# Kernel optimization log

Hardware: AMD Instinct MI355X
Metric: run time of the kernel (lower is better)

## Reference

```python
import jax, jax.numpy as jnp
import numpy as np
import math

EMBED_DIM = 1024
NUM_HEADS = 16
HEAD_DIM = EMBED_DIM // NUM_HEADS
WINDOW_SIZE = 32  # one-sided; full window = 2*w+1 = 65
SCALING = math.sqrt(HEAD_DIM)


def setup_inputs() -> dict:
    key = jax.random.key(0)
    ks = jax.random.split(key, 9)
    B, S, E = 2, 2048, EMBED_DIM
    s = 1.0 / math.sqrt(E)
    inp = {
        "hidden_states": jax.random.normal(ks[0], (B, S, E), dtype=jnp.float32),
        "q_w": jax.random.uniform(ks[1], (E, E), jnp.float32, -s, s),
        "q_b": jax.random.uniform(ks[2], (E,), jnp.float32, -s, s),
        "k_w": jax.random.uniform(ks[3], (E, E), jnp.float32, -s, s),
        "k_b": jax.random.uniform(ks[4], (E,), jnp.float32, -s, s),
        "v_w": jax.random.uniform(ks[5], (E, E), jnp.float32, -s, s),
        "v_b": jax.random.uniform(ks[6], (E,), jnp.float32, -s, s),
        "o_w": jax.random.uniform(ks[7], (E, E), jnp.float32, -s, s),
        "o_b": jax.random.uniform(ks[8], (E,), jnp.float32, -s, s),
    }
    return inp


def reference(hidden_states, q_w, q_b, k_w, k_b, v_w, v_b, o_w, o_b):
    B, S, E = hidden_states.shape
    H, D, w = NUM_HEADS, HEAD_DIM, WINDOW_SIZE
    W = 2 * w + 1

    q = hidden_states @ q_w.T + q_b
    k = hidden_states @ k_w.T + k_b
    v = hidden_states @ v_w.T + v_b

    # [B, H, S, D]
    q = q.reshape(B, S, H, D).transpose(0, 2, 1, 3)
    k = k.reshape(B, S, H, D).transpose(0, 2, 1, 3)
    v = v.reshape(B, S, H, D).transpose(0, 2, 1, 3)

    # zero-pad seq dim by w on each side (matches F.pad value=0); padded keys
    # contribute score 0 (NOT -inf) exactly like the original unfold scheme.
    k_pad = jnp.pad(k, ((0, 0), (0, 0), (w, w), (0, 0)))
    v_pad = jnp.pad(v, ((0, 0), (0, 0), (w, w), (0, 0)))

    # window gather indices: query i sees padded positions i..i+2w (orig i-w..i+w)
    idx = jnp.arange(S)[:, None] + jnp.arange(W)[None, :]  # [S, W]
    k_slice = k_pad[:, :, idx]  # [B, H, S, W, D]
    v_slice = v_pad[:, :, idx]  # [B, H, S, W, D]

    score = jnp.einsum('bhsd,bhswd->bhsw', q, k_slice) / SCALING
    p = jax.nn.softmax(score, axis=-1)
    attn = jnp.einsum('bhsw,bhswd->bhsd', p, v_slice)

    attn = attn.transpose(0, 2, 1, 3).reshape(B, S, E)
    return attn @ o_w.T + o_b
```

## Files before the change

kernel.cpp:

```cpp
#include <hip/hip_runtime.h>
#include <math.h>

typedef _Float16 h16;
typedef _Float16 h8 __attribute__((ext_vector_type(8)));
typedef float f32x4 __attribute__((ext_vector_type(4)));

__device__ inline void gl2lds16(const void* g, void* l) {
  __builtin_amdgcn_global_load_lds(
      (const __attribute__((address_space(1))) void*)g,
      (__attribute__((address_space(3))) void*)l, 16, 0, 0);
}

#define VMCNT(N) asm volatile("s_waitcnt vmcnt(" #N ")" ::: "memory")

__global__ __launch_bounds__(256) void f2h_all(
    const float* __restrict__ hs, const float* __restrict__ w0,
    const float* __restrict__ w1, const float* __restrict__ w2,
    const float* __restrict__ w3, h16* __restrict__ dst, int hsN) {
  int i = (blockIdx.x * 256 + threadIdx.x) * 8;
  const int tot = hsN + 4 * 1048576;
  if (i >= tot) return;
  const float* src;
  int off;
  if (i < hsN) {
    src = hs; off = i;
  } else {
    int k = i - hsN;
    int seg = k >> 20;
    off = k & 1048575;
    src = seg == 0 ? w0 : seg == 1 ? w1 : seg == 2 ? w2 : w3;
  }
  float4 a = *(const float4*)(src + off);
  float4 b = *(const float4*)(src + off + 4);
  h8 o;
  o[0] = (h16)a.x; o[1] = (h16)a.y; o[2] = (h16)a.z; o[3] = (h16)a.w;
  o[4] = (h16)b.x; o[5] = (h16)b.y; o[6] = (h16)b.z; o[7] = (h16)b.w;
  *(h8*)(dst + i) = o;
}

__global__ __launch_bounds__(256) void qkv97(
    const h16* __restrict__ A, const h16* __restrict__ Bw,
    const float* __restrict__ qb, const float* __restrict__ kb,
    const float* __restrict__ vb, h16* __restrict__ qo, h16* __restrict__ ko,
    h16* __restrict__ vo) {
  __shared__ __align__(16) h16 Ash[128 * 32];
  __shared__ __align__(16) h16 Bsh[128 * 32];
  __shared__ __align__(16) h16 Csh[128 * 136];

  const int tid = threadIdx.x;
  const int wid = tid >> 6, lane = tid & 63;
  const int lr = lane & 15, lg = lane >> 4;
  const int wr = wid >> 1, wc = wid & 1;
  const int srow = tid >> 2;
  const int csw = ((tid & 3) ^ ((srow >> 1) & 3)) * 8;

  const int wg = (blockIdx.x & 7) * 96 + (blockIdx.x >> 3);
  const int bm = wg & 31, bn = wg >> 5;
  const int row0 = bm * 128, col0 = bn * 128;

  const h16* Ag = A + (size_t)row0 * 1024;
  const h16* Bg = Bw + (size_t)col0 * 1024;

  auto ldf = [&](const h16* base, int row) -> h8 {
    return *(const h8*)(base + row * 32 + (lg ^ ((row >> 1) & 3)) * 8);
  };

  f32x4 acc[4][4] = {};

  for (int t = 0; t < 32; ++t) {
    const int kof = t * 32 + csw;
    gl2lds16(Ag + (size_t)srow * 1024 + kof, &Ash[(wid * 16) * 32]);
    gl2lds16(Ag + (size_t)(64 + srow) * 1024 + kof, &Ash[(64 + wid * 16) * 32]);
    gl2lds16(Bg + (size_t)srow * 1024 + kof, &Bsh[(wid * 16) * 32]);
    gl2lds16(Bg + (size_t)(64 + srow) * 1024 + kof, &Bsh[(64 + wid * 16) * 32]);
    __syncthreads();
    h8 af[4], bf[4];
#pragma unroll
    for (int m = 0; m < 4; ++m) af[m] = ldf(Ash, wr * 64 + m * 16 + lr);
#pragma unroll
    for (int n = 0; n < 4; ++n) bf[n] = ldf(Bsh, wc * 64 + n * 16 + lr);
    __builtin_amdgcn_s_setprio(1);
#pragma unroll
    for (int m = 0; m < 4; ++m)
#pragma unroll
      for (int n = 0; n < 4; ++n)
        acc[m][n] =
            __builtin_amdgcn_mfma_f32_16x16x32_f16(af[m], bf[n], acc[m][n], 0, 0, 0);
    __builtin_amdgcn_s_setprio(0);
    __syncthreads();
  }

  const int tsel = bn >> 3;
  const int colseg = (bn & 7) * 128;
  const float* bp = tsel == 0 ? qb : (tsel == 1 ? kb : vb);
  h16* outp = tsel == 0 ? qo : (tsel == 1 ? ko : vo);

#pragma unroll
  for (int n = 0; n < 4; ++n) {
    const int ccol = wc * 64 + n * 16 + lr;
    const float bv = bp[colseg + ccol];
#pragma unroll
    for (int m = 0; m < 4; ++m)
#pragma unroll
      for (int j = 0; j < 4; ++j)
        Csh[(wr * 64 + m * 16 + lg * 4 + j) * 136 + ccol] =
            (h16)(acc[m][n][j] + bv);
  }
  __syncthreads();
#pragma unroll
  for (int p = 0; p < 8; ++p) {
    const int idx = p * 256 + tid;
    const int r = idx >> 4, c = idx & 15;
    h8 v = *(const h8*)&Csh[r * 136 + c * 8];
    *(h8*)&outp[(size_t)(row0 + r) * 1024 + colseg + c * 8] = v;
  }
}

__global__ __launch_bounds__(64) void oproj1w(const h16* __restrict__ A,
                                              const h16* __restrict__ Bw,
                                              const float* __restrict__ b0,
                                              float* __restrict__ Cf) {
  __shared__ __align__(16) h16 Ash[2][32][64];
  __shared__ __align__(16) h16 Bsh[2][128][64];

  const int lane = threadIdx.x;
  const int lr = lane & 15, lg = lane >> 4;
  const int srw = lane >> 3;
  const int csw = ((lane & 7) ^ (srw & 7)) * 8;

  const int wg = (blockIdx.x & 7) * 128 + (blockIdx.x >> 3);
  const int bm = wg & 127, bn = wg >> 7;
  const int row0 = bm * 32, col0 = bn * 128;

  const h16* Ag = A + (size_t)row0 * 1024;
  const h16* Bg = Bw + (size_t)col0 * 1024;

  auto stage = [&](int t, int bi) {
    const int kof = t * 64 + csw;
#pragma unroll
    for (int rs = 0; rs < 32; rs += 8)
      gl2lds16(Ag + (size_t)(rs + srw) * 1024 + kof, &Ash[bi][rs][0]);
#pragma unroll
    for (int rs = 0; rs < 128; rs += 8)
      gl2lds16(Bg + (size_t)(rs + srw) * 1024 + kof, &Bsh[bi][rs][0]);
  };
  auto ldf = [&](const h16* base, int row, int kk) -> h8 {
    return *(const h8*)(base + row * 64 + ((kk * 4 + lg) ^ (row & 7)) * 8);
  };

  f32x4 acc[2][8] = {};

  stage(0, 0);
  for (int t = 0; t < 16; ++t) {
    if (t + 1 < 16) {
      stage(t + 1, (t + 1) & 1);
      VMCNT(20);
    } else {
      VMCNT(0);
    }
    const h16* Ar = &Ash[t & 1][0][0];
    const h16* Br = &Bsh[t & 1][0][0];
    h8 af[2][2], bf[8][2];
#pragma unroll
    for (int m = 0; m < 2; ++m)
#pragma unroll
      for (int kk = 0; kk < 2; ++kk) af[m][kk] = ldf(Ar, m * 16 + lr, kk);
#pragma unroll
    for (int n = 0; n < 8; ++n)
#pragma unroll
      for (int kk = 0; kk < 2; ++kk) bf[n][kk] = ldf(Br, n * 16 + lr, kk);
    __builtin_amdgcn_s_setprio(1);
#pragma unroll
    for (int m = 0; m < 2; ++m)
#pragma unroll
      for (int n = 0; n < 8; ++n)
#pragma unroll
        for (int kk = 0; kk < 2; ++kk)
          acc[m][n] = __builtin_amdgcn_mfma_f32_16x16x32_f16(af[m][kk], bf[n][kk],
                                                             acc[m][n], 0, 0, 0);
    __builtin_amdgcn_s_setprio(0);
  }

#pragma unroll
  for (int n = 0; n < 8; ++n) {
    const int cidx = col0 + n * 16 + lr;
    const float bv = b0[cidx];
#pragma unroll
    for (int m = 0; m < 2; ++m)
#pragma unroll
      for (int j = 0; j < 4; ++j) {
        const int r = row0 + m * 16 + lg * 4 + j;
        Cf[(size_t)r * 1024 + cidx] = acc[m][n][j] + bv;
      }
  }
}

__global__ __launch_bounds__(256) void swattn(const h16* __restrict__ Q,
                                              const h16* __restrict__ K,
                                              const h16* __restrict__ V,
                                              h16* __restrict__ O) {
  __shared__ __align__(16) h16 Ksh[128 * 72];
  __shared__ __align__(16) h16 Vsh[64 * 136];
  __shared__ __align__(16) h16 Psh[4][16 * 136];

  const int qb0 = blockIdx.x * 64;
  const int bh = blockIdx.y;
  const int b = bh >> 4, h = bh & 15;
  const int tid = threadIdx.x;
  const int wave = tid >> 6, lane = tid & 63;
  const int lr = lane & 15, lg = lane >> 4;

  const h16* Qb = Q + (size_t)b * 2048 * 1024 + h * 64;
  const h16* Kb = K + (size_t)b * 2048 * 1024 + h * 64;
  const h16* Vb = V + (size_t)b * 2048 * 1024 + h * 64;

#pragma unroll
  for (int i = 0; i < 4; ++i) {
    const int c = tid * 4 + i;
    const int row = c >> 3, c8 = c & 7;
    const int t = qb0 - 32 + row;
    h8 kv, vv;
    if (t >= 0 && t < 2048) {
      kv = *(const h8*)&Kb[(size_t)t * 1024 + c8 * 8];
      vv = *(const h8*)&Vb[(size_t)t * 1024 + c8 * 8];
    } else {
#pragma unroll
      for (int j = 0; j < 8; ++j) { kv[j] = (h16)0.f; vv[j] = (h16)0.f; }
    }
    *(h8*)&Ksh[row * 72 + c8 * 8] = kv;
#pragma unroll
    for (int j = 0; j < 8; ++j) Vsh[(c8 * 8 + j) * 136 + row] = vv[j];
  }
  __syncthreads();

  const int qrow = qb0 + wave * 16 + lr;
  h8 qa[2];
#pragma unroll
  for (int kk = 0; kk < 2; ++kk)
    qa[kk] = *(const h8*)&Qb[(size_t)qrow * 1024 + kk * 32 + lg * 8];

  f32x4 sacc[8] = {};
#pragma unroll
  for (int n = 0; n < 8; ++n)
#pragma unroll
    for (int kk = 0; kk < 2; ++kk) {
      h8 kb = *(const h8*)&Ksh[(n * 16 + lr) * 72 + kk * 32 + lg * 8];
      sacc[n] = __builtin_amdgcn_mfma_f32_16x16x32_f16(qa[kk], kb, sacc[n], 0, 0, 0);
    }

  float p[8][4];
#pragma unroll
  for (int j = 0; j < 4; ++j) {
    const int wrow = wave * 16 + lg * 4 + j;
    float mx = -1e30f;
#pragma unroll
    for (int n = 0; n < 8; ++n) {
      const int d = n * 16 + lr - wrow;
      float s = (d < 0 || d > 64) ? -1e30f : sacc[n][j] * 0.125f;
      p[n][j] = s;
      mx = fmaxf(mx, s);
    }
#pragma unroll
    for (int off = 1; off < 16; off <<= 1) mx = fmaxf(mx, __shfl_xor(mx, off, 64));
    float sum = 0.f;
#pragma unroll
    for (int n = 0; n < 8; ++n) {
      const float e = __expf(p[n][j] - mx);
      p[n][j] = e;
      sum += e;
    }
#pragma unroll
    for (int off = 1; off < 16; off <<= 1) sum += __shfl_xor(sum, off, 64);
    const float inv = 1.f / sum;
#pragma unroll
    for (int n = 0; n < 8; ++n) p[n][j] *= inv;
  }

#pragma unroll
  for (int n = 0; n < 8; ++n)
#pragma unroll
    for (int j = 0; j < 4; ++j)
      Psh[wave][(lg * 4 + j) * 136 + n * 16 + lr] = (h16)p[n][j];
  __syncthreads();

  f32x4 oacc[4] = {};
#pragma unroll
  for (int kk = 0; kk < 4; ++kk) {
    h8 pa = *(const h8*)&Psh[wave][lr * 136 + kk * 32 + lg * 8];
#pragma unroll
    for (int n = 0; n < 4; ++n) {
      h8 vb = *(const h8*)&Vsh[(n * 16 + lr) * 136 + kk * 32 + lg * 8];
      oacc[n] = __builtin_amdgcn_mfma_f32_16x16x32_f16(pa, vb, oacc[n], 0, 0, 0);
    }
  }

#pragma unroll
  for (int n = 0; n < 4; ++n)
#pragma unroll
    for (int j = 0; j < 4; ++j) {
      const int s = qb0 + wave * 16 + lg * 4 + j;
      const int d = n * 16 + lr;
      O[((size_t)b * 2048 + s) * 1024 + h * 64 + d] = (h16)oacc[n][j];
    }
}

extern "C" void kernel_launch(void* const* d_in, const int* in_sizes, int n_in,
                              void* d_out, int out_size, void* d_ws, size_t ws_size,
                              hipStream_t stream) {
  const float* hs = (const float*)d_in[0];
  const float* qw = (const float*)d_in[1];
  const float* qb = (const float*)d_in[2];
  const float* kw = (const float*)d_in[3];
  const float* kb = (const float*)d_in[4];
  const float* vw = (const float*)d_in[5];
  const float* vb = (const float*)d_in[6];
  const float* ow = (const float*)d_in[7];
  const float* ob = (const float*)d_in[8];

  const int M = in_sizes[0] / 1024;

  h16* hsH = (h16*)d_ws;
  h16* wqkv = hsH + (size_t)M * 1024;
  h16* woH = wqkv + (size_t)3072 * 1024;
  h16* qH = woH + (size_t)1024 * 1024;
  h16* kH = qH + (size_t)M * 1024;
  h16* vH = kH + (size_t)M * 1024;
  h16* attnH = vH + (size_t)M * 1024;

  const int tot = M * 1024 + 4 * 1048576;
  f2h_all<<<(tot / 8 + 255) / 256, 256, 0, stream>>>(hs, qw, kw, vw, ow, hsH,
                                                     M * 1024);

  qkv97<<<768, 256, 0, stream>>>(hsH, wqkv, qb, kb, vb, qH, kH, vH);

  swattn<<<dim3(32, M / 2048 * 16), 256, 0, stream>>>(qH, kH, vH, attnH);

  oproj1w<<<1024, 64, 0, stream>>>(attnH, woH, ob, (float*)d_out);
}
```

Before: 86.65 us.

## Double-buffer QKV GEMM loads and rewrite output projection as 4-wave tiles

Measured after the change: 92.59 us. +6.8%, slower.

```diff
diff --git a/kernel.cpp b/kernel.cpp
--- a/kernel.cpp
+++ b/kernel.cpp
@@ -9,6 +9,12 @@
   __builtin_amdgcn_global_load_lds(
       (const __attribute__((address_space(1))) void*)g,
       (__attribute__((address_space(3))) void*)l, 16, 0, 0);
+}
+
+__device__ inline void barrier_raw() {
+  asm volatile("" ::: "memory");
+  __builtin_amdgcn_s_barrier();
+  asm volatile("" ::: "memory");
 }
 
 #define VMCNT(N) asm volatile("s_waitcnt vmcnt(" #N ")" ::: "memory")
@@ -38,14 +44,15 @@
   *(h8*)(dst + i) = o;
 }
 
-__global__ __launch_bounds__(256) void qkv97(
+__global__ __launch_bounds__(256, 4) void qkv9(
     const h16* __restrict__ A, const h16* __restrict__ Bw,
     const float* __restrict__ qb, const float* __restrict__ kb,
     const float* __restrict__ vb, h16* __restrict__ qo, h16* __restrict__ ko,
     h16* __restrict__ vo) {
-  __shared__ __align__(16) h16 Ash[128 * 32];
-  __shared__ __align__(16) h16 Bsh[128 * 32];
-  __shared__ __align__(16) h16 Csh[128 * 136];
+  __shared__ __align__(16) char smem[128 * 136 * 2];
+  h16* Abuf = (h16*)smem;
+  h16* Bbuf = Abuf + 2 * 128 * 32;
+  h16* Csh = (h16*)smem;
 
   const int tid = threadIdx.x;
   const int wid = tid >> 6, lane = tid & 63;
@@ -61,24 +68,37 @@
   const h16* Ag = A + (size_t)row0 * 1024;
   const h16* Bg = Bw + (size_t)col0 * 1024;
 
+  auto stage = [&](int t, int bi) {
+    const int kof = t * 32 + csw;
+    h16* Ad = Abuf + bi * 128 * 32;
+    h16* Bd = Bbuf + bi * 128 * 32;
+    gl2lds16(Ag + (size_t)srow * 1024 + kof, Ad + (wid * 16) * 32);
+    gl2lds16(Ag + (size_t)(64 + srow) * 1024 + kof, Ad + (64 + wid * 16) * 32);
+    gl2lds16(Bg + (size_t)srow * 1024 + kof, Bd + (wid * 16) * 32);
+    gl2lds16(Bg + (size_t)(64 + srow) * 1024 + kof, Bd + (64 + wid * 16) * 32);
+  };
   auto ldf = [&](const h16* base, int row) -> h8 {
     return *(const h8*)(base + row * 32 + (lg ^ ((row >> 1) & 3)) * 8);
   };
 
   f32x4 acc[4][4] = {};
 
+  stage(0, 0);
   for (int t = 0; t < 32; ++t) {
-    const int kof = t * 32 + csw;
-    gl2lds16(Ag + (size_t)srow * 1024 + kof, &Ash[(wid * 16) * 32]);
-    gl2lds16(Ag + (size_t)(64 + srow) * 1024 + kof, &Ash[(64 + wid * 16) * 32]);
-    gl2lds16(Bg + (size_t)srow * 1024 + kof, &Bsh[(wid * 16) * 32]);
-    gl2lds16(Bg + (size_t)(64 + srow) * 1024 + kof, &Bsh[(64 + wid * 16) * 32]);
-    __syncthreads();
+    if (t < 31) {
+      stage(t + 1, (t + 1) & 1);
+      VMCNT(4);
+    } else {
+      VMCNT(0);
+    }
+    barrier_raw();
+    const h16* Ar = Abuf + (t & 1) * 128 * 32;
+    const h16* Br = Bbuf + (t & 1) * 128 * 32;
     h8 af[4], bf[4];
 #pragma unroll
-    for (int m = 0; m < 4; ++m) af[m] = ldf(Ash, wr * 64 + m * 16 + lr);
-#pragma unroll
-    for (int n = 0; n < 4; ++n) bf[n] = ldf(Bsh, wc * 64 + n * 16 + lr);
+    for (int m = 0; m < 4; ++m) af[m] = ldf(Ar, wr * 64 + m * 16 + lr);
+#pragma unroll
+    for (int n = 0; n < 4; ++n) bf[n] = ldf(Br, wc * 64 + n * 16 + lr);
     __builtin_amdgcn_s_setprio(1);
 #pragma unroll
     for (int m = 0; m < 4; ++m)
@@ -87,7 +107,7 @@
         acc[m][n] =
             __builtin_amdgcn_mfma_f32_16x16x32_f16(af[m], bf[n], acc[m][n], 0, 0, 0);
     __builtin_amdgcn_s_setprio(0);
-    __syncthreads();
+    barrier_raw();
   }
 
   const int tsel = bn >> 3;
@@ -106,7 +126,7 @@
         Csh[(wr * 64 + m * 16 + lg * 4 + j) * 136 + ccol] =
             (h16)(acc[m][n][j] + bv);
   }
-  __syncthreads();
+  barrier_raw();
 #pragma unroll
   for (int p = 0; p < 8; ++p) {
     const int idx = p * 256 + tid;
@@ -116,80 +136,75 @@
   }
 }
 
-__global__ __launch_bounds__(64) void oproj1w(const h16* __restrict__ A,
+__global__ __launch_bounds__(256) void oproj9(const h16* __restrict__ A,
                                               const h16* __restrict__ Bw,
                                               const float* __restrict__ b0,
                                               float* __restrict__ Cf) {
-  __shared__ __align__(16) h16 Ash[2][32][64];
-  __shared__ __align__(16) h16 Bsh[2][128][64];
-
-  const int lane = threadIdx.x;
+  __shared__ __align__(16) h16 Abuf[2][64][32];
+  __shared__ __align__(16) h16 Bbuf[2][128][32];
+
+  const int tid = threadIdx.x;
+  const int wid = tid >> 6, lane = tid & 63;
   const int lr = lane & 15, lg = lane >> 4;
-  const int srw = lane >> 3;
-  const int csw = ((lane & 7) ^ (srw & 7)) * 8;
-
-  const int wg = (blockIdx.x & 7) * 128 + (blockIdx.x >> 3);
-  const int bm = wg & 127, bn = wg >> 7;
-  const int row0 = bm * 32, col0 = bn * 128;
+  const int wr = wid >> 1, wc = wid & 1;
+  const int srow = tid >> 2;
+  const int csw = ((tid & 3) ^ ((srow >> 1) & 3)) * 8;
+
+  const int wg = (blockIdx.x & 7) * 64 + (blockIdx.x >> 3);
+  const int bm = wg & 63, bn = wg >> 6;
+  const int row0 = bm * 64, col0 = bn * 128;
 
   const h16* Ag = A + (size_t)row0 * 1024;
   const h16* Bg = Bw + (size_t)col0 * 1024;
 
   auto stage = [&](int t, int bi) {
-    const int kof = t * 64 + csw;
-#pragma unroll
-    for (int rs = 0; rs < 32; rs += 8)
-      gl2lds16(Ag + (size_t)(rs + srw) * 1024 + kof, &Ash[bi][rs][0]);
-#pragma unroll
-    for (int rs = 0; rs < 128; rs += 8)
-      gl2lds16(Bg + (size_t)(rs + srw) * 1024 + kof, &Bsh[bi][rs][0]);
+    const int kof = t * 32 + csw;
+    gl2lds16(Ag + (size_t)srow * 1024 + kof, &Abuf[bi][wid * 16][0]);
+    gl2lds16(Bg + (size_t)srow * 1024 + kof, &Bbuf[bi][wid * 16][0]);
+    gl2lds16(Bg + (size_t)(64 + srow) * 1024 + kof, &Bbuf[bi][64 + wid * 16][0]);
   };
-  auto ldf = [&](const h16* base, int row, int kk) -> h8 {
-    return *(const h8*)(base + row * 64 + ((kk * 4 + lg) ^ (row & 7)) * 8);
+  auto ldf = [&](const h16* base, int row) -> h8 {
+    return *(const h8*)(base + row * 32 + (lg ^ ((row >> 1) & 3)) * 8);
   };
 
-  f32x4 acc[2][8] = {};
+  f32x4 acc[2][4] = {};
 
   stage(0, 0);
-  for (int t = 0; t < 16; ++t) {
-    if (t + 1 < 16) {
+  for (int t = 0; t < 32; ++t) {
+    if (t < 31) {
       stage(t + 1, (t + 1) & 1);
-      VMCNT(20);
+      VMCNT(3);
     } else {
       VMCNT(0);
     }
-    const h16* Ar = &Ash[t & 1][0][0];
-    const h16* Br = &Bsh[t & 1][0][0];
-    h8 af[2][2], bf[8][2];
+    barrier_raw();
+    const h16* Ar = &Abuf[t & 1][0][0];
+    const h16* Br = &Bbuf[t & 1][0][0];
+    h8 af[2], bf[4];
+#pragma unroll
+    for (int m = 0; m < 2; ++m) af[m] = ldf(Ar, wr * 32 + m * 16 + lr);
+#pragma unroll
+    for (int n = 0; n < 4; ++n) bf[n] = ldf(Br, wc * 64 + n * 16 + lr);
+    __builtin_amdgcn_s_setprio(1);
 #pragma unroll
     for (int m = 0; m < 2; ++m)
 #pragma unroll
-      for (int kk = 0; kk < 2; ++kk) af[m][kk] = ldf(Ar, m * 16 + lr, kk);
-#pragma unroll
-    for (int n = 0; n < 8; ++n)
-#pragma unroll
-      for (int kk = 0; kk < 2; ++kk) bf[n][kk] = ldf(Br, n * 16 + lr, kk);
-    __builtin_amdgcn_s_setprio(1);
+      for (int n = 0; n < 4; ++n)
+        acc[m][n] =
+            __builtin_amdgcn_mfma_f32_16x16x32_f16(af[m], bf[n], acc[m][n], 0, 0, 0);
+    __builtin_amdgcn_s_setprio(0);
+    barrier_raw();
+  }
+
+#pragma unroll
+  for (int n = 0; n < 4; ++n) {
+    const int cidx = col0 + wc * 64 + n * 16 + lr;
+    const float bv = b0[cidx];
 #pragma unroll
     for (int m = 0; m < 2; ++m)
 #pragma unroll
-      for (int n = 0; n < 8; ++n)
-#pragma unroll
-        for (int kk = 0; kk < 2; ++kk)
-          acc[m][n] = __builtin_amdgcn_mfma_f32_16x16x32_f16(af[m][kk], bf[n][kk],
-                                                             acc[m][n], 0, 0, 0);
-    __builtin_amdgcn_s_setprio(0);
-  }
-
-#pragma unroll
-  for (int n = 0; n < 8; ++n) {
-    const int cidx = col0 + n * 16 + lr;
-    const float bv = b0[cidx];
-#pragma unroll
-    for (int m = 0; m < 2; ++m)
-#pragma unroll
       for (int j = 0; j < 4; ++j) {
-        const int r = row0 + m * 16 + lg * 4 + j;
+        const int r = row0 + wr * 32 + m * 16 + lg * 4 + j;
         Cf[(size_t)r * 1024 + cidx] = acc[m][n][j] + bv;
       }
   }
@@ -331,9 +346,9 @@
   f2h_all<<<(tot / 8 + 255) / 256, 256, 0, stream>>>(hs, qw, kw, vw, ow, hsH,
                                                      M * 1024);
 
-  qkv97<<<768, 256, 0, stream>>>(hsH, wqkv, qb, kb, vb, qH, kH, vH);
+  qkv9<<<768, 256, 0, stream>>>(hsH, wqkv, qb, kb, vb, qH, kH, vH);
 
   swattn<<<dim3(32, M / 2048 * 16), 256, 0, stream>>>(qH, kH, vH, attnH);
 
-  oproj1w<<<1024, 64, 0, stream>>>(attnH, woH, ob, (float*)d_out);
-}
+  oproj9<<<512, 256, 0, stream>>>(attnH, woH, ob, (float*)d_out);
+}
```
